# Performance work log

Measured on AMD Instinct MI355X. Metric: run time of the kernel, lower is better.

Reference implementation:

```python
import jax, jax.numpy as jnp
import numpy as np


def setup_inputs() -> dict:
    key = jax.random.key(0)
    k1, k2 = jax.random.split(key, 2)
    N, C, H, W, G = 64, 256, 56, 56, 32
    x = jax.random.normal(k1, (N, C, H, W), dtype=jnp.float32)
    # fc: Linear(batch_size*2 -> group)
    fc_w = jax.random.normal(k2, (G, 2 * N), dtype=jnp.float32) * 0.05
    fc_b = jnp.zeros((G,), dtype=jnp.float32)
    # affine params (1, C, 1, 1), init ones/zeros as in the module
    weight = jnp.ones((1, C, 1, 1), dtype=jnp.float32)
    bias = jnp.zeros((1, C, 1, 1), dtype=jnp.float32)
    return {"x": x, "fc_w": fc_w, "fc_b": fc_b, "weight": weight, "bias": bias, "group": G}


def reference(x, fc_w, fc_b, weight, bias, group):
    eps = 1e-5
    N, C, H, W = x.shape
    hw = H * W
    # --- routing features: per-channel mean/var over (N is kept, reduce HW) ---
    # torch: x_ = x.transpose(0,1).view(C,N,HW); mean/var(-1) with unbiased var (ddof=1)
    mean_cn = jnp.mean(x, axis=(2, 3)).T           # [C, N]
    var_cn = jnp.var(x, axis=(2, 3), ddof=1).T     # [C, N]
    s = jnp.concatenate([mean_cn, var_cn], axis=1)  # [C, 2N]
    probs = jax.nn.softmax(s @ fc_w.T + fc_b, axis=1)  # [C, G]
    g = jnp.argmax(probs, axis=1)                  # [C] channel -> group
    onehot = jax.nn.one_hot(g, group, dtype=x.dtype)  # [C, G]
    # --- per-(sample, group) mean/var via segment reduce expressed as GEMM ---
    s1 = jnp.sum(x, axis=(2, 3))        # [N, C]
    s2 = jnp.sum(x * x, axis=(2, 3))    # [N, C]
    S1 = s1 @ onehot                    # [N, G]
    S2 = s2 @ onehot                    # [N, G]
    cnt = jnp.sum(onehot, axis=0) * hw  # [G] elements per (n, g)
    mean_g = S1 / jnp.maximum(cnt, 1.0)                          # [N, G]
    # unbiased variance (torch .var default): (sum_sq - n*mean^2)/(n-1)
    var_g = (S2 - S1 * mean_g) / jnp.maximum(cnt - 1.0, 1.0)     # [N, G]
    # empty groups are skipped in the original; no channel maps to them, so
    # the guarded denominators only prevent NaNs and never affect outputs.
    mean_c = mean_g[:, g]  # [N, C] gather per-channel stats
    var_c = var_g[:, g]    # [N, C]
    xn = (x - mean_c[:, :, None, None]) * jax.lax.rsqrt(var_c + eps)[:, :, None, None]
    return xn * weight + bias
```

## Files before the change

kernel.cpp:

```cpp
#include <hip/hip_runtime.h>

constexpr int N_  = 64;
constexpr int C_  = 256;
constexpr int HW_ = 56 * 56;
constexpr int NV_ = HW_ / 4;
constexpr int G_  = 32;
constexpr int NC_ = N_ * C_;
constexpr float EPS_ = 1e-5f;

typedef float f32x4 __attribute__((ext_vector_type(4)));

__global__ __launch_bounds__(256) void k_sums(const float* __restrict__ x,
                                              float* __restrict__ s1,
                                              float* __restrict__ s2) {
    const int wave = threadIdx.x >> 6;
    const int lane = threadIdx.x & 63;
    const int nc = blockIdx.x * 4 + wave;
    const f32x4* xp = reinterpret_cast<const f32x4*>(x + (size_t)nc * HW_);
    f32x4 v[12];
    #pragma unroll
    for (int k = 0; k < 12; ++k) v[k] = xp[lane + k * 64];
    f32x4 vt;
    const bool tail = lane < 16;
    if (tail) vt = xp[768 + lane];
    float a = 0.f, b = 0.f;
    #pragma unroll
    for (int k = 0; k < 12; ++k) {
        a += (v[k].x + v[k].y) + (v[k].z + v[k].w);
        b += (v[k].x * v[k].x + v[k].y * v[k].y) + (v[k].z * v[k].z + v[k].w * v[k].w);
    }
    if (tail) {
        a += (vt.x + vt.y) + (vt.z + vt.w);
        b += (vt.x * vt.x + vt.y * vt.y) + (vt.z * vt.z + vt.w * vt.w);
    }
    #pragma unroll
    for (int off = 32; off; off >>= 1) {
        a += __shfl_down(a, off, 64);
        b += __shfl_down(b, off, 64);
    }
    if (lane == 0) { s1[nc] = a; s2[nc] = b; }
}

__global__ __launch_bounds__(64) void k_logits(const float* __restrict__ s1,
                                               const float* __restrict__ s2,
                                               const float* __restrict__ fc_w,
                                               const float* __restrict__ fc_b,
                                               int* __restrict__ gidx) {
    const int c = blockIdx.x;
    const int t = threadIdx.x;
    const int g = t & 31, half = t >> 5;
    const float inv_hw  = 1.f / (float)HW_;
    const float inv_hw1 = 1.f / (float)(HW_ - 1);
    const float* wg = fc_w + g * (2 * N_);
    float acc = half ? 0.f : fc_b[g];
    const int n0 = half * 32;
    #pragma unroll 8
    for (int n = n0; n < n0 + 32; ++n) {
        const float v1 = s1[n * C_ + c];
        const float v2 = s2[n * C_ + c];
        const float m  = v1 * inv_hw;
        const float vr = (v2 - v1 * m) * inv_hw1;
        acc += m * wg[n] + vr * wg[N_ + n];
    }
    acc += __shfl_down(acc, 32, 64);
    __shared__ float lg[G_];
    if (half == 0) lg[g] = acc;
    __syncthreads();
    if (t == 0) {
        float best = lg[0];
        int bi = 0;
        for (int g2 = 1; g2 < G_; ++g2) {
            const float v = lg[g2];
            if (v > best) { best = v; bi = g2; }
        }
        gidx[c] = bi;
    }
}

__global__ __launch_bounds__(256) void k_norm_g(const float* __restrict__ x,
                                                const float* __restrict__ s1,
                                                const float* __restrict__ s2,
                                                const int* __restrict__ gidx,
                                                const float* __restrict__ weight,
                                                const float* __restrict__ bias,
                                                float* __restrict__ out) {
    const int b    = blockIdx.x;
    const int t    = threadIdx.x;
    const int w    = t >> 6;
    const int lane = t & 63;
    const int nc   = b * 4 + w;
    const int n    = nc >> 8;
    const int c    = nc & (C_ - 1);

    const f32x4* xp = reinterpret_cast<const f32x4*>(x) + (size_t)nc * NV_;
    f32x4 v[12];
    #pragma unroll
    for (int k = 0; k < 12; ++k) v[k] = xp[lane + k * 64];
    f32x4 vt;
    const bool tail = lane < 16;
    if (tail) vt = xp[768 + lane];

    __shared__ float r1[C_], r2[C_];
    __shared__ int   gi[C_];
    __shared__ float mg[G_], ig[G_];
    r1[t] = s1[n * C_ + t];
    r2[t] = s2[n * C_ + t];
    gi[t] = gidx[t];
    __syncthreads();
    if (t < G_) {
        float A = 0.f, B = 0.f; int k = 0;
        for (int cc = 0; cc < C_; ++cc)
            if (gi[cc] == t) { A += r1[cc]; B += r2[cc]; ++k; }
        const float cf = (float)k * (float)HW_;
        const float m  = A / fmaxf(cf, 1.f);
        const float vr = (B - A * m) / fmaxf(cf - 1.f, 1.f);
        mg[t] = m;
        ig[t] = rsqrtf(vr + EPS_);
    }
    __syncthreads();

    const int g = gi[c];
    const float sc = ig[g] * weight[c];
    const float sh = bias[c] - mg[g] * sc;
    f32x4* op = reinterpret_cast<f32x4*>(out) + (size_t)nc * NV_;
    #pragma unroll
    for (int k = 0; k < 12; ++k)
        __builtin_nontemporal_store(v[k] * sc + sh, op + lane + k * 64);
    if (tail)
        __builtin_nontemporal_store(vt * sc + sh, op + 768 + lane);
}

extern "C" void kernel_launch(void* const* d_in, const int* in_sizes, int n_in,
                              void* d_out, int out_size, void* d_ws, size_t ws_size,
                              hipStream_t stream) {
    const float* x      = (const float*)d_in[0];
    const float* fc_w   = (const float*)d_in[1];
    const float* fc_b   = (const float*)d_in[2];
    const float* weight = (const float*)d_in[3];
    const float* bias   = (const float*)d_in[4];
    float* outp = (float*)d_out;

    float* ws    = (float*)d_ws;
    float* s1    = ws;
    float* s2    = ws + NC_;
    int*   gidxg = (int*)(ws + 2 * NC_);

    k_sums  <<<NC_ / 4, 256, 0, stream>>>(x, s1, s2);
    k_logits<<<C_,       64, 0, stream>>>(s1, s2, fc_w, fc_b, gidxg);
    k_norm_g<<<NC_ / 4, 256, 0, stream>>>(x, s1, s2, gidxg, weight, bias, outp);
}
```

Measured before the change: 128.4 us.

## Move group stats into a per-sample mid kernel emitting per-channel scale/shift

Replaces the logits kernel and the per-block group-statistics work in the normalization kernel with a middle kernel. It runs one block per sample, recomputes the routing argmax redundantly in each block, computes group mean/var once, and writes per-(n,c) scale and shift. The final kernel then only loads scale/shift and applies an affine transform. This removes the serial 256-iteration group reduction and the extra syncs that each of the 4096 normalization blocks used to repeat. The cost is that the logits computation is now done 64 times with 32-wide register accumulators.

```diff
diff --git a/kernel.cpp b/kernel.cpp
--- a/kernel.cpp
+++ b/kernel.cpp
@@ -41,76 +41,65 @@
     if (lane == 0) { s1[nc] = a; s2[nc] = b; }
 }
 
-__global__ __launch_bounds__(64) void k_logits(const float* __restrict__ s1,
-                                               const float* __restrict__ s2,
-                                               const float* __restrict__ fc_w,
-                                               const float* __restrict__ fc_b,
-                                               int* __restrict__ gidx) {
-    const int c = blockIdx.x;
+__global__ __launch_bounds__(256) void k_mid(const float* __restrict__ s1,
+                                             const float* __restrict__ s2,
+                                             const float* __restrict__ fc_w,
+                                             const float* __restrict__ fc_b,
+                                             const float* __restrict__ weight,
+                                             const float* __restrict__ bias,
+                                             float* __restrict__ scale,
+                                             float* __restrict__ shift) {
+    const int n = blockIdx.x;
     const int t = threadIdx.x;
-    const int g = t & 31, half = t >> 5;
+
+    __shared__ float wT[2 * N_ * G_];
+    __shared__ float bL[G_];
+    __shared__ float r1s[C_], r2s[C_];
+    __shared__ int   gi[C_];
+    __shared__ float mg[G_], ig[G_];
+
+    for (int i = t; i < 2 * N_ * G_; i += 256) {
+        const int nn = i >> 5, g = i & (G_ - 1);
+        wT[i] = fc_w[g * (2 * N_) + nn];
+    }
+    if (t < G_) bL[t] = fc_b[t];
+    __syncthreads();
+
     const float inv_hw  = 1.f / (float)HW_;
     const float inv_hw1 = 1.f / (float)(HW_ - 1);
-    const float* wg = fc_w + g * (2 * N_);
-    float acc = half ? 0.f : fc_b[g];
-    const int n0 = half * 32;
-    #pragma unroll 8
-    for (int n = n0; n < n0 + 32; ++n) {
-        const float v1 = s1[n * C_ + c];
-        const float v2 = s2[n * C_ + c];
+
+    float acc[G_];
+    #pragma unroll
+    for (int g = 0; g < G_; ++g) acc[g] = bL[g];
+    float myr1 = 0.f, myr2 = 0.f;
+
+    for (int nn = 0; nn < N_; ++nn) {
+        const float v1 = s1[nn * C_ + t];
+        const float v2 = s2[nn * C_ + t];
         const float m  = v1 * inv_hw;
         const float vr = (v2 - v1 * m) * inv_hw1;
-        acc += m * wg[n] + vr * wg[N_ + n];
+        if (nn == n) { myr1 = v1; myr2 = v2; }
+        const float* w1 = &wT[nn * G_];
+        const float* w2 = &wT[(N_ + nn) * G_];
+        #pragma unroll
+        for (int g = 0; g < G_; ++g)
+            acc[g] += m * w1[g] + vr * w2[g];
     }
-    acc += __shfl_down(acc, 32, 64);
-    __shared__ float lg[G_];
-    if (half == 0) lg[g] = acc;
+
+    float best = acc[0]; int bi = 0;
+    #pragma unroll
+    for (int g = 1; g < G_; ++g)
+        if (acc[g] > best) { best = acc[g]; bi = g; }
+
+    gi[t]  = bi;
+    r1s[t] = myr1;
+    r2s[t] = myr2;
     __syncthreads();
-    if (t == 0) {
-        float best = lg[0];
-        int bi = 0;
-        for (int g2 = 1; g2 < G_; ++g2) {
-            const float v = lg[g2];
-            if (v > best) { best = v; bi = g2; }
-        }
-        gidx[c] = bi;
-    }
-}
 
-__global__ __launch_bounds__(256) void k_norm_g(const float* __restrict__ x,
-                                                const float* __restrict__ s1,
-                                                const float* __restrict__ s2,
-                                                const int* __restrict__ gidx,
-                                                const float* __restrict__ weight,
-                                                const float* __restrict__ bias,
-                                                float* __restrict__ out) {
-    const int b    = blockIdx.x;
-    const int t    = threadIdx.x;
-    const int w    = t >> 6;
-    const int lane = t & 63;
-    const int nc   = b * 4 + w;
-    const int n    = nc >> 8;
-    const int c    = nc & (C_ - 1);
-
-    const f32x4* xp = reinterpret_cast<const f32x4*>(x) + (size_t)nc * NV_;
-    f32x4 v[12];
-    #pragma unroll
-    for (int k = 0; k < 12; ++k) v[k] = xp[lane + k * 64];
-    f32x4 vt;
-    const bool tail = lane < 16;
-    if (tail) vt = xp[768 + lane];
-
-    __shared__ float r1[C_], r2[C_];
-    __shared__ int   gi[C_];
-    __shared__ float mg[G_], ig[G_];
-    r1[t] = s1[n * C_ + t];
-    r2[t] = s2[n * C_ + t];
-    gi[t] = gidx[t];
-    __syncthreads();
     if (t < G_) {
         float A = 0.f, B = 0.f; int k = 0;
         for (int cc = 0; cc < C_; ++cc)
-            if (gi[cc] == t) { A += r1[cc]; B += r2[cc]; ++k; }
+            if (gi[cc] == t) { A += r1s[cc]; B += r2s[cc]; ++k; }
         const float cf = (float)k * (float)HW_;
         const float m  = A / fmaxf(cf, 1.f);
         const float vr = (B - A * m) / fmaxf(cf - 1.f, 1.f);
@@ -119,10 +108,29 @@
     }
     __syncthreads();
 
-    const int g = gi[c];
-    const float sc = ig[g] * weight[c];
-    const float sh = bias[c] - mg[g] * sc;
-    f32x4* op = reinterpret_cast<f32x4*>(out) + (size_t)nc * NV_;
+    const int g = gi[t];
+    const float sc = ig[g] * weight[t];
+    scale[n * C_ + t] = sc;
+    shift[n * C_ + t] = bias[t] - mg[g] * sc;
+}
+
+__global__ __launch_bounds__(256) void k_norm(const float* __restrict__ x,
+                                              const float* __restrict__ scale,
+                                              const float* __restrict__ shift,
+                                              float* __restrict__ out) {
+    const int wave = threadIdx.x >> 6;
+    const int lane = threadIdx.x & 63;
+    const int nc = blockIdx.x * 4 + wave;
+    const float sc = scale[nc];
+    const float sh = shift[nc];
+    const f32x4* xp = reinterpret_cast<const f32x4*>(x + (size_t)nc * HW_);
+    f32x4* op = reinterpret_cast<f32x4*>(out + (size_t)nc * HW_);
+    f32x4 v[12];
+    #pragma unroll
+    for (int k = 0; k < 12; ++k) v[k] = xp[lane + k * 64];
+    f32x4 vt;
+    const bool tail = lane < 16;
+    if (tail) vt = xp[768 + lane];
     #pragma unroll
     for (int k = 0; k < 12; ++k)
         __builtin_nontemporal_store(v[k] * sc + sh, op + lane + k * 64);
@@ -143,9 +151,10 @@
     float* ws    = (float*)d_ws;
     float* s1    = ws;
     float* s2    = ws + NC_;
-    int*   gidxg = (int*)(ws + 2 * NC_);
+    float* scale = ws + 2 * NC_;
+    float* shift = ws + 3 * NC_;
 
-    k_sums  <<<NC_ / 4, 256, 0, stream>>>(x, s1, s2);
-    k_logits<<<C_,       64, 0, stream>>>(s1, s2, fc_w, fc_b, gidxg);
-    k_norm_g<<<NC_ / 4, 256, 0, stream>>>(x, s1, s2, gidxg, weight, bias, outp);
+    k_sums<<<NC_ / 4, 256, 0, stream>>>(x, s1, s2);
+    k_mid <<<N_,      256, 0, stream>>>(s1, s2, fc_w, fc_b, weight, bias, scale, shift);
+    k_norm<<<NC_ / 4, 256, 0, stream>>>(x, scale, shift, outp);
 }
```

Measured after the change: 151.6 us. 18.0% more time.
